# Kernel optimization log

Measured on AMD Instinct MI355X. Metric: run time of the kernel, lower is better.

The kernel has to match this reference:

```python
import jax, jax.numpy as jnp
import numpy as np

IN_CH, OUT_CH, HEADS = 256, 128, 4
DIM_HEAD = OUT_CH // HEADS  # 32 (module overrides dim_head = out_ch // heads)
R = 16  # reduce_size
EPS = 1e-5


def _conv3d(x, w, groups=1, pad=0):
    return jax.lax.conv_general_dilated(
        x, w, (1, 1, 1), [(pad, pad)] * 3,
        dimension_numbers=('NCDHW', 'OIDHW', 'NCDHW'),
        feature_group_count=groups)


def _dwsep(x, wd, wp):
    # depthwise 3x3x3 (groups=C) then pointwise 1x1x1, both bias-free
    y = _conv3d(x, wd, groups=x.shape[1], pad=1)
    return _conv3d(y, wp)


def _bn(x, g, b):
    # training-mode BatchNorm3d: biased batch stats over (N, D, H, W)
    m = x.mean(axis=(0, 2, 3, 4), keepdims=True)
    v = x.var(axis=(0, 2, 3, 4), keepdims=True)
    return (x - m) * jax.lax.rsqrt(v + EPS) * g.reshape(1, -1, 1, 1, 1) + b.reshape(1, -1, 1, 1, 1)


def _interp1(x, axis, out_len):
    in_len = x.shape[axis]
    if in_len == out_len:
        return x
    pos = jnp.arange(out_len, dtype=x.dtype) * ((in_len - 1) / (out_len - 1))  # align_corners=True
    lo = jnp.clip(jnp.floor(pos).astype(jnp.int32), 0, in_len - 1)
    hi = jnp.clip(lo + 1, 0, in_len - 1)
    w = pos - lo.astype(x.dtype)
    shp = [1] * x.ndim
    shp[axis] = out_len
    w = w.reshape(shp)
    return jnp.take(x, lo, axis=axis) * (1 - w) + jnp.take(x, hi, axis=axis) * w


def _interp3(x, size):
    for ax, s in zip((2, 3, 4), size):
        x = _interp1(x, ax, s)
    return x


def _rel_index(h, w, d):
    c = np.stack(np.meshgrid(np.arange(h), np.arange(w), np.arange(d), indexing='ij')).reshape(3, -1)
    rel = (c[:, :, None] - c[:, None, :]).transpose(1, 2, 0).astype(np.int64)
    rel[:, :, 0] += h - 1
    rel[:, :, 1] += w - 1
    rel[:, :, 0] *= 2 * h - 1
    idx = rel.sum(-1)
    # faithful to torch: negative indices wrap around the table
    return idx % ((2 * h - 1) * (2 * w - 1) * (2 * d - 1))


def _rel_bias(table, h, w, d, H, W, D, heads):
    idx = _rel_index(h, w, d)
    bias = table[idx.reshape(-1)].reshape(h, w, d, h * w, -1)
    bias = jnp.repeat(bias, H // h, axis=0)
    bias = jnp.repeat(bias, W // w, axis=1)
    bias = jnp.repeat(bias, D // d, axis=2)
    return bias.reshape(H * W * D, h * w * d, heads).transpose(2, 0, 1)[None]  # [1,heads,Nq,Nk]


def setup_inputs() -> dict:
    key = jax.random.key(0)
    ks = jax.random.split(key, 12)
    n = lambda k, s: jax.random.normal(k, s, dtype=jnp.float32)
    return {
        'x1': n(ks[0], (1, IN_CH, 8, 8, 8)),
        'x2': n(ks[1], (1, OUT_CH, 16, 16, 16)),
        'w_ch': n(ks[2], (OUT_CH, IN_CH, 1, 1, 1)) * 0.05,
        'b_ch': jnp.zeros((OUT_CH,), jnp.float32),
        'gamma_l': jnp.ones((IN_CH,), jnp.float32), 'beta_l': jnp.zeros((IN_CH,), jnp.float32),
        'gamma_h': jnp.ones((OUT_CH,), jnp.float32), 'beta_h': jnp.zeros((OUT_CH,), jnp.float32),
        'gamma2': jnp.ones((OUT_CH,), jnp.float32), 'beta2': jnp.zeros((OUT_CH,), jnp.float32),
        'kv_dw': n(ks[3], (IN_CH, 1, 3, 3, 3)) * 0.05,
        'kv_pw': n(ks[4], (2 * OUT_CH, IN_CH, 1, 1, 1)) * 0.05,
        'q_dw': n(ks[5], (OUT_CH, 1, 3, 3, 3)) * 0.05,
        'q_pw': n(ks[6], (OUT_CH, OUT_CH, 1, 1, 1)) * 0.05,
        'out_dw': n(ks[7], (OUT_CH, 1, 3, 3, 3)) * 0.05,
        'out_pw': n(ks[8], (OUT_CH, OUT_CH, 1, 1, 1)) * 0.05,
        'w_mlp': n(ks[9], (OUT_CH, OUT_CH, 1, 1, 1)) * 0.05,
        'rel_table': n(ks[10], ((2 * R - 1) ** 3, HEADS)) * 0.02,
    }


def reference(x1, x2, w_ch, b_ch, gamma_l, beta_l, gamma_h, beta_h, gamma2, beta2,
              kv_dw, kv_pw, q_dw, q_pw, out_dw, out_pw, w_mlp, rel_table):
    B, C, H, W, D = x1.shape
    _, _, HH, WH, DH = x2.shape
    residue = _interp3(_conv3d(x1, w_ch) + b_ch.reshape(1, -1, 1, 1, 1), (HH, WH, DH))
    x1n = _bn(x1, gamma_l, beta_l)
    x2n = _bn(x2, gamma_h, beta_h)
    k, v = jnp.split(_dwsep(x1n, kv_dw, kv_pw), 2, axis=1)
    q = _dwsep(x2n, q_dw, q_pw)
    if H != R:
        k = _interp3(k, (R, R, R))
        v = _interp3(v, (R, R, R))

    def heads_split(t, h, w_, d):
        # channel layout is (dim_head, heads)
        t = t.reshape(B, DIM_HEAD, HEADS, h, w_, d)
        return t.transpose(0, 2, 3, 4, 5, 1).reshape(B, HEADS, h * w_ * d, DIM_HEAD)

    qh = heads_split(q, HH, WH, DH)
    kh = heads_split(k, R, R, R)
    vh = heads_split(v, R, R, R)
    attn = jnp.einsum('bhid,bhjd->bhij', qh, kh)
    attn = attn + _rel_bias(rel_table, R, R, R, HH, WH, DH, HEADS)
    attn = jax.nn.softmax(attn * (DIM_HEAD ** -0.5), axis=-1)  # note: bias is scaled too, as in source
    o = jnp.einsum('bhij,bhjd->bhid', attn, vh)
    o = o.reshape(B, HEADS, HH, WH, DH, DIM_HEAD).transpose(0, 5, 1, 2, 3, 4).reshape(B, OUT_CH, HH, WH, DH)
    o = _dwsep(o, out_dw, out_pw)
    o = o + residue
    res2 = o
    o = jax.nn.relu(_bn(o, gamma2, beta2))
    o = _conv3d(o, w_mlp)
    return o + res2
```

## Files before the change

kernel.cpp:

```cpp
#include <hip/hip_runtime.h>
#include <hip/hip_bf16.h>

using f32x4  = __attribute__((ext_vector_type(4))) float;
using bf16x8 = __attribute__((ext_vector_type(8))) short;
using i32x4  = __attribute__((ext_vector_type(4))) int;

static constexpr float SCALE = 0.17677669529663687f;
static constexpr float L2E   = 1.4426950408889634f;
static constexpr float SL    = SCALE * L2E;

__device__ inline int cvtpk(float lo, float hi) {
  int r;
  asm("v_cvt_pk_bf16_f32 %0,%1,%2" : "=v"(r) : "v"(lo), "v"(hi));
  return r;
}

__device__ inline void bred2(float& s, float& ss) {
  #pragma unroll
  for (int off = 32; off; off >>= 1) {
    s  += __shfl_down(s, off, 64);
    ss += __shfl_down(ss, off, 64);
  }
  __shared__ float as_[4], ass_[4];
  int wid = threadIdx.x >> 6;
  if ((threadIdx.x & 63) == 0) { as_[wid] = s; ass_[wid] = ss; }
  __syncthreads();
  s  = as_[0] + as_[1] + as_[2] + as_[3];
  ss = ass_[0] + ass_[1] + ass_[2] + ass_[3];
}

__global__ __launch_bounds__(256) void bnstat_both_kernel(
    const float* __restrict__ x1, const float* __restrict__ x2,
    const float* __restrict__ gl, const float* __restrict__ bl,
    const float* __restrict__ gh, const float* __restrict__ bh,
    float* __restrict__ ab_l, float* __restrict__ ab_h) {
  int b = blockIdx.x;
  const float* src; const float *gamma, *beta; float* ab; int S, C, c;
  if (b < 256) { c = b;       src = x1 + (size_t)c * 512;  S = 512;  C = 256; gamma = gl; beta = bl; ab = ab_l; }
  else         { c = b - 256; src = x2 + (size_t)c * 4096; S = 4096; C = 128; gamma = gh; beta = bh; ab = ab_h; }
  float s = 0.f, ss = 0.f;
  for (int i = threadIdx.x; i < S; i += 256) { float v = src[i]; s += v; ss = fmaf(v, v, ss); }
  bred2(s, ss);
  if (threadIdx.x == 0) {
    float inv = 1.0f / (float)S;
    float m   = s * inv;
    float var = ss * inv - m * m;
    float a   = gamma[c] * rsqrtf(var + 1e-5f);
    ab[c]     = a;
    ab[C + c] = beta[c] - m * a;
  }
}

template<bool AFF>
__device__ inline void dw_body(
    const float* __restrict__ in, const float* __restrict__ w,
    const float* __restrict__ ab, float* __restrict__ out,
    int n, int nn, int n3, int C, int t) {
  int c = t / n3, s = t - c * n3;
  int z = s / nn, r = s - z * nn, y = r / n, x = r - y * n;
  const float* src = in + (size_t)c * n3;
  const float* wc  = w + c * 27;
  float a = 1.f, b = 0.f;
  if (AFF) { a = ab[c]; b = ab[C + c]; }
  float acc = 0.f;
  #pragma unroll
  for (int kd = 0; kd < 3; kd++) {
    int zz = z + kd - 1;
    if (zz < 0 || zz >= n) continue;
    #pragma unroll
    for (int kh = 0; kh < 3; kh++) {
      int yy = y + kh - 1;
      if (yy < 0 || yy >= n) continue;
      #pragma unroll
      for (int kw = 0; kw < 3; kw++) {
        int xx = x + kw - 1;
        if (xx < 0 || xx >= n) continue;
        float v = src[(zz * n + yy) * n + xx];
        if (AFF) v = fmaf(v, a, b);
        acc = fmaf(v, wc[kd * 9 + kh * 3 + kw], acc);
      }
    }
  }
  out[t] = acc;
}

__global__ __launch_bounds__(256) void stageA_kernel(
    const float* __restrict__ x1, const float* __restrict__ x2,
    const float* __restrict__ w_ch, const float* __restrict__ b_ch,
    const float* __restrict__ kv_dw, const float* __restrict__ q_dw,
    const float* __restrict__ ab_l, const float* __restrict__ ab_h,
    float* __restrict__ res8, float* __restrict__ kvdw, float* __restrict__ qdw) {
  int b = blockIdx.x;
  if (b < 128) {
    int oc0 = (b >> 1) * 2;
    int s   = (b & 1) * 256 + threadIdx.x;
    float a0 = 0.f, a1 = 0.f;
    const float* w0 = w_ch + (size_t)oc0 * 256;
    const float* w1 = w0 + 256;
    #pragma unroll 8
    for (int ic = 0; ic < 256; ic++) {
      float x = x1[(size_t)ic * 512 + s];
      a0 = fmaf(w0[ic], x, a0);
      a1 = fmaf(w1[ic], x, a1);
    }
    res8[(size_t)oc0 * 512 + s]       = a0 + b_ch[oc0];
    res8[(size_t)(oc0 + 1) * 512 + s] = a1 + b_ch[oc0 + 1];
  } else if (b < 640) {
    dw_body<true>(x1, kv_dw, ab_l, kvdw, 8, 64, 512, 256, (b - 128) * 256 + threadIdx.x);
  } else {
    dw_body<true>(x2, q_dw, ab_h, qdw, 16, 256, 4096, 128, (b - 640) * 256 + threadIdx.x);
  }
}

__device__ inline void icoef8(int o, int& lo, int& hi, float& w) {
  float p = (float)o * (7.0f / 15.0f);
  int l = (int)floorf(p);
  if (l > 7) l = 7;
  int h = l + 1 > 7 ? 7 : l + 1;
  w  = p - (float)l;
  lo = l; hi = h;
}

__device__ inline float trilin8(const float* __restrict__ p,
                                int z0, int z1, float wz,
                                int y0, int y1, float wy,
                                int x0, int x1, float wx) {
  float c00 = p[(z0*8+y0)*8+x0]*(1.f-wx) + p[(z0*8+y0)*8+x1]*wx;
  float c01 = p[(z0*8+y1)*8+x0]*(1.f-wx) + p[(z0*8+y1)*8+x1]*wx;
  float c10 = p[(z1*8+y0)*8+x0]*(1.f-wx) + p[(z1*8+y0)*8+x1]*wx;
  float c11 = p[(z1*8+y1)*8+x0]*(1.f-wx) + p[(z1*8+y1)*8+x1]*wx;
  float c0 = c00*(1.f-wy) + c01*wy;
  float c1 = c10*(1.f-wy) + c11*wy;
  return c0*(1.f-wz) + c1*wz;
}

__global__ __launch_bounds__(512) void stageB_kernel(
    const float* __restrict__ kvdw, const float* __restrict__ kv_pw,
    const float* __restrict__ qdw, const float* __restrict__ q_pw,
    const float* __restrict__ res8,
    unsigned short* __restrict__ Kb, unsigned short* __restrict__ Vt,
    unsigned short* __restrict__ Qpk, float* __restrict__ r16) {
  __shared__ float sm[2][512];
  int b = blockIdx.x;
  int tid = threadIdx.x;
  if (b < 128) {
    int kc0 = b * 2;
    int s = tid;
    float a0 = 0.f, a1 = 0.f;
    const float* w0 = kv_pw + (size_t)kc0 * 256;
    const float* w1 = w0 + 256;
    #pragma unroll 8
    for (int ic = 0; ic < 256; ic++) {
      float x = kvdw[(size_t)ic * 512 + s];
      a0 = fmaf(w0[ic], x, a0);
      a1 = fmaf(w1[ic], x, a1);
    }
    sm[0][s] = a0; sm[1][s] = a1;
    __syncthreads();
    #pragma unroll
    for (int r = 0; r < 16; r++) {
      int u  = r * 512 + tid;
      int cl = u >> 12, j = u & 4095;
      int z = j >> 8, y = (j >> 4) & 15, x = j & 15;
      int z0,z1,y0,y1,x0,x1; float wz,wy,wx;
      icoef8(z, z0, z1, wz); icoef8(y, y0, y1, wy); icoef8(x, x0, x1, wx);
      float val = trilin8(sm[cl], z0, z1, wz, y0, y1, wy, x0, x1, wx);
      __hip_bfloat16 bv = __float2bfloat16(val);
      unsigned short us = *reinterpret_cast<unsigned short*>(&bv);
      int kc = kc0 + cl;
      int c  = kc & 127;
      int head = c & 3, dh = c >> 2;
      if (kc < 128) Kb[((size_t)(head << 12) + j) * 32 + dh] = us;
      else          Vt[((size_t)(head * 32) + dh) * 4096 + j] = us;
    }
  } else if (b < 256) {
    int bb   = b - 128;
    int head = bb >> 5;
    int r2   = bb & 31;
    int dh0  = (r2 >> 3) * 8;
    int i    = (r2 & 7) * 512 + tid;
    float acc[8];
    #pragma unroll
    for (int e = 0; e < 8; e++) acc[e] = 0.f;
    #pragma unroll 4
    for (int ic = 0; ic < 128; ic++) {
      float x = qdw[(size_t)ic * 4096 + i];
      #pragma unroll
      for (int e = 0; e < 8; e++)
        acc[e] = fmaf(q_pw[(size_t)((dh0 + e) * 4 + head) * 128 + ic], x, acc[e]);
    }
    i32x4 pk = { cvtpk(acc[0], acc[1]), cvtpk(acc[2], acc[3]),
                 cvtpk(acc[4], acc[5]), cvtpk(acc[6], acc[7]) };
    *reinterpret_cast<i32x4*>(Qpk + ((size_t)(head << 12) + i) * 32 + dh0) = pk;
  } else {
    int t = (b - 256) * 512 + tid;
    int s = t & 4095, c = t >> 12;
    int z = s >> 8, y = (s >> 4) & 15, x = s & 15;
    int z0,z1,y0,y1,x0,x1; float wz,wy,wx;
    icoef8(z, z0, z1, wz); icoef8(y, y0, y1, wy); icoef8(x, x0, x1, wx);
    r16[t] = trilin8(res8 + c * 512, z0, z1, wz, y0, y1, wy, x0, x1, wx);
  }
}

__global__ __launch_bounds__(512, 4) void attn_mfma_kernel(
    const unsigned short* __restrict__ Qpk, const unsigned short* __restrict__ Kb,
    const unsigned short* __restrict__ Vt, const float* __restrict__ table,
    float* __restrict__ part_o, float* __restrict__ part_m, float* __restrict__ part_l) {
  __shared__ float lut[992];
  __shared__ unsigned short kvs[2][4096];

  int head = blockIdx.x >> 8;
  int rem  = blockIdx.x & 255;
  int qg   = rem >> 3;
  int ksb  = rem & 7;
  int tid  = threadIdx.x;

  for (int u = tid; u < 991; u += 512) {
    int p = (u < 15) ? (u - 15 + 29791) : (u - 15);
    lut[u] = table[p * 4 + head] * SL;
  }

  int w    = tid >> 6;
  int lane = tid & 63;
  int qrow = lane & 15;
  int g    = lane >> 4;
  int i    = qg * 128 + w * 16 + qrow;
  int iz = i >> 8, iy = (i >> 4) & 15, ix = i & 15;
  int lanebase = iz * 31 + iy + ix;

  bf16x8 qf = *(const bf16x8*)(Qpk + ((size_t)(head << 12) + i) * 32 + g * 8);

  const unsigned short* Kh = Kb + (size_t)head * 4096 * 32;
  const unsigned short* Vh = Vt + (size_t)head * 32 * 4096;

  int kt0 = ksb * 16;

  const unsigned short* src;
  size_t sstride;
  if (tid < 256) {
    int key = tid >> 2, s = tid & 3;
    int gp  = s ^ ((key >> 1) & 3);
    src = Kh + (size_t)(kt0 * 32 + key) * 32 + gp * 8;
    sstride = 32 * 32;
  } else {
    int tt = tid - 256;
    int dh = tt >> 2, s = tt & 3;
    int gp = s ^ ((dh >> 1) & 3);
    src = Vh + (size_t)dh * 4096 + kt0 * 32 + gp * 8;
    sstride = 32;
  }
  int t8 = tid * 8;

  int sw    = (qrow >> 1) & 3;
  int k0off = qrow * 32 + ((g ^ sw) * 8);
  int k1off = k0off + 512;
  int v0off = 2048 + k0off;
  int v1off = v0off + 512;

  {
    bf16x8 s0 = *(const bf16x8*)src; src += sstride;
    *(bf16x8*)(&kvs[0][t8]) = s0;
  }
  __syncthreads();

  f32x4 zero = {0.f, 0.f, 0.f, 0.f};
  f32x4 accO0 = zero, accO1 = zero;
  float m2 = -1e30f, lpart = 0.f;
  int cur = 0;

  for (int ktl = 0; ktl < 16; ktl++) {
    int kt = kt0 + ktl;
    bf16x8 stg;
    if (ktl < 15) { stg = *(const bf16x8*)src; src += sstride; }

    bf16x8 kf0 = *(const bf16x8*)(&kvs[cur][k0off]);
    bf16x8 kf1 = *(const bf16x8*)(&kvs[cur][k1off]);
    bf16x8 vf0 = *(const bf16x8*)(&kvs[cur][v0off]);
    bf16x8 vf1 = *(const bf16x8*)(&kvs[cur][v1off]);

    f32x4 accA = __builtin_amdgcn_mfma_f32_16x16x32_bf16(kf0, qf, zero, 0, 0, 0);
    f32x4 accB = __builtin_amdgcn_mfma_f32_16x16x32_bf16(kf1, qf, zero, 0, 0, 0);

    int z0 = kt >> 3, y0 = (kt << 1) & 15;
    int Cc = 495 - 31 * z0 - y0;
    const float* lp = &lut[lanebase + Cc - 4 * g - 4];
    float l0 = lp[0], l1 = lp[1], l2 = lp[2], l3 = lp[3], l4 = lp[4];

    float t0 = fmaf(accA[0], SL, l4);
    float t1 = fmaf(accA[1], SL, l3);
    float t2 = fmaf(accA[2], SL, l2);
    float t3 = fmaf(accA[3], SL, l1);
    float t4 = fmaf(accB[0], SL, l3);
    float t5 = fmaf(accB[1], SL, l2);
    float t6 = fmaf(accB[2], SL, l1);
    float t7 = fmaf(accB[3], SL, l0);

    float cm = fmaxf(fmaxf(fmaxf(t0, t1), fmaxf(t2, t3)),
                     fmaxf(fmaxf(t4, t5), fmaxf(t6, t7)));
    cm = fmaxf(cm, __shfl_xor(cm, 16, 64));
    cm = fmaxf(cm, __shfl_xor(cm, 32, 64));

    if (__any(cm > m2 + 8.f)) {
      float mn   = fmaxf(m2, cm);
      float corr = exp2f(m2 - mn);
      m2 = mn;
      lpart *= corr;
      accO0[0] *= corr; accO0[1] *= corr; accO0[2] *= corr; accO0[3] *= corr;
      accO1[0] *= corr; accO1[1] *= corr; accO1[2] *= corr; accO1[3] *= corr;
    }

    float p0 = exp2f(t0 - m2), p1 = exp2f(t1 - m2);
    float p2 = exp2f(t2 - m2), p3 = exp2f(t3 - m2);
    float p4 = exp2f(t4 - m2), p5 = exp2f(t5 - m2);
    float p6 = exp2f(t6 - m2), p7 = exp2f(t7 - m2);
    lpart += ((p0 + p1) + (p2 + p3)) + ((p4 + p5) + (p6 + p7));

    int w0 = cvtpk(p0, p1), w1 = cvtpk(p2, p3);
    int w2 = cvtpk(p4, p5), w3 = cvtpk(p6, p7);
    int srcA = ((g & 1) << 5) + qrow;
    int srcB = srcA + 16;
    int x0 = __shfl(w0, srcA, 64), x1 = __shfl(w1, srcA, 64);
    int x2 = __shfl(w2, srcA, 64), x3 = __shfl(w3, srcA, 64);
    int y0s = __shfl(w0, srcB, 64), y1s = __shfl(w1, srcB, 64);
    int y2s = __shfl(w2, srcB, 64), y3s = __shfl(w3, srcB, 64);
    bool thi = (g >> 1) != 0;
    union { i32x4 i4; bf16x8 s8; } up;
    up.i4 = (i32x4){ thi ? x2 : x0, thi ? x3 : x1,
                     thi ? y2s : y0s, thi ? y3s : y1s };

    accO0 = __builtin_amdgcn_mfma_f32_16x16x32_bf16(vf0, up.s8, accO0, 0, 0, 0);
    accO1 = __builtin_amdgcn_mfma_f32_16x16x32_bf16(vf1, up.s8, accO1, 0, 0, 0);

    if (ktl < 15) *(bf16x8*)(&kvs[cur ^ 1][t8]) = stg;
    __syncthreads();
    cur ^= 1;
  }

  float lsum = lpart + __shfl_xor(lpart, 16, 64);
  lsum += __shfl_xor(lsum, 32, 64);

  int base = head * 8 + ksb;
  if (g == 0) {
    part_m[base * 4096 + i] = m2;
    part_l[base * 4096 + i] = lsum;
  }
  #pragma unroll
  for (int r = 0; r < 4; r++) {
    part_o[(size_t)(base * 32 + 4 * g + r) * 4096 + i]      = accO0[r];
    part_o[(size_t)(base * 32 + 16 + 4 * g + r) * 4096 + i] = accO1[r];
  }
}

__global__ __launch_bounds__(256) void attn_reduce_kernel(
    const float* __restrict__ part_o, const float* __restrict__ part_m,
    const float* __restrict__ part_l, float* __restrict__ o_sp) {
  int t = blockIdx.x * 256 + threadIdx.x;
  int i = t & 4095, head = t >> 12;
  float mk[8], mx = -1e30f;
  #pragma unroll
  for (int ks = 0; ks < 8; ks++) { mk[ks] = part_m[(head*8+ks)*4096 + i]; mx = fmaxf(mx, mk[ks]); }
  float c[8], L = 0.f;
  #pragma unroll
  for (int ks = 0; ks < 8; ks++) {
    c[ks] = exp2f(mk[ks] - mx);
    L = fmaf(c[ks], part_l[(head*8+ks)*4096 + i], L);
  }
  float invL = 1.f / L;
  #pragma unroll
  for (int d = 0; d < 32; d++) {
    float acc = 0.f;
    #pragma unroll
    for (int ks = 0; ks < 8; ks++)
      acc = fmaf(c[ks], part_o[(size_t)((head*8+ks)*32 + d) * 4096 + i], acc);
    o_sp[(size_t)(d * 4 + head) * 4096 + i] = acc * invL;
  }
}

__global__ __launch_bounds__(256) void dw_out_kernel(
    const float* __restrict__ in, const float* __restrict__ w, float* __restrict__ out) {
  dw_body<false>(in, w, nullptr, out, 16, 256, 4096, 128, blockIdx.x * 256 + threadIdx.x);
}

__global__ __launch_bounds__(256) void pw_out_kernel(
    const float* __restrict__ in, const float* __restrict__ w,
    const float* __restrict__ r16, float* __restrict__ res2,
    float* __restrict__ sums) {
  __shared__ float red[4][2][2];
  int oc0 = (blockIdx.x >> 3) * 2;
  int sb  = blockIdx.x & 7;
  int s0  = (sb * 256 + threadIdx.x) * 2;
  float a00 = 0.f, a01 = 0.f, a10 = 0.f, a11 = 0.f;
  const float* w0 = w + (size_t)oc0 * 128;
  const float* w1 = w0 + 128;
  #pragma unroll 8
  for (int ic = 0; ic < 128; ic++) {
    float xa = in[(size_t)ic * 4096 + s0];
    float xb = in[(size_t)ic * 4096 + s0 + 1];
    float wv0 = w0[ic], wv1 = w1[ic];
    a00 = fmaf(wv0, xa, a00); a01 = fmaf(wv0, xb, a01);
    a10 = fmaf(wv1, xa, a10); a11 = fmaf(wv1, xb, a11);
  }
  size_t ob0 = (size_t)oc0 * 4096 + s0;
  size_t ob1 = ob0 + 4096;
  float r00 = a00 + r16[ob0],     r01 = a01 + r16[ob0 + 1];
  float r10 = a10 + r16[ob1],     r11 = a11 + r16[ob1 + 1];
  res2[ob0] = r00; res2[ob0 + 1] = r01;
  res2[ob1] = r10; res2[ob1 + 1] = r11;
  float s_0 = r00 + r01, q_0 = fmaf(r00, r00, r01 * r01);
  float s_1 = r10 + r11, q_1 = fmaf(r10, r10, r11 * r11);
  #pragma unroll
  for (int off = 32; off; off >>= 1) {
    s_0 += __shfl_down(s_0, off, 64); q_0 += __shfl_down(q_0, off, 64);
    s_1 += __shfl_down(s_1, off, 64); q_1 += __shfl_down(q_1, off, 64);
  }
  int wid = threadIdx.x >> 6;
  if ((threadIdx.x & 63) == 0) {
    red[wid][0][0] = s_0; red[wid][0][1] = q_0;
    red[wid][1][0] = s_1; red[wid][1][1] = q_1;
  }
  __syncthreads();
  if (threadIdx.x < 2) {
    int o = threadIdx.x;
    float st = red[0][o][0] + red[1][o][0] + red[2][o][0] + red[3][o][0];
    float qt = red[0][o][1] + red[1][o][1] + red[2][o][1] + red[3][o][1];
    sums[(oc0 + o) * 8 + sb]        = st;
    sums[1024 + (oc0 + o) * 8 + sb] = qt;
  }
}

__global__ __launch_bounds__(256) void pw_mlp_kernel(
    const float* __restrict__ res2, const float* __restrict__ w,
    const float* __restrict__ gamma2, const float* __restrict__ beta2,
    const float* __restrict__ sums, float* __restrict__ out) {
  __shared__ float A[128], Bb[128];
  if (threadIdx.x < 128) {
    int c = threadIdx.x;
    float s = 0.f, q = 0.f;
    #pragma unroll
    for (int sb = 0; sb < 8; sb++) { s += sums[c * 8 + sb]; q += sums[1024 + c * 8 + sb]; }
    float m   = s * (1.0f / 4096.0f);
    float var = q * (1.0f / 4096.0f) - m * m;
    float a   = gamma2[c] * rsqrtf(var + 1e-5f);
    A[c]  = a;
    Bb[c] = beta2[c] - m * a;
  }
  __syncthreads();
  int oc0 = (blockIdx.x >> 3) * 2;
  int sb  = blockIdx.x & 7;
  int s0  = (sb * 256 + threadIdx.x) * 2;
  float a00 = 0.f, a01 = 0.f, a10 = 0.f, a11 = 0.f;
  const float* w0 = w + (size_t)oc0 * 128;
  const float* w1 = w0 + 128;
  #pragma unroll 8
  for (int ic = 0; ic < 128; ic++) {
    float aa = A[ic], bb = Bb[ic];
    float xa = fmaxf(fmaf(res2[(size_t)ic * 4096 + s0], aa, bb), 0.f);
    float xb = fmaxf(fmaf(res2[(size_t)ic * 4096 + s0 + 1], aa, bb), 0.f);
    float wv0 = w0[ic], wv1 = w1[ic];
    a00 = fmaf(wv0, xa, a00); a01 = fmaf(wv0, xb, a01);
    a10 = fmaf(wv1, xa, a10); a11 = fmaf(wv1, xb, a11);
  }
  size_t ob0 = (size_t)oc0 * 4096 + s0;
  size_t ob1 = ob0 + 4096;
  out[ob0]     = a00 + res2[ob0];
  out[ob0 + 1] = a01 + res2[ob0 + 1];
  out[ob1]     = a10 + res2[ob1];
  out[ob1 + 1] = a11 + res2[ob1 + 1];
}

extern "C" void kernel_launch(void* const* d_in, const int* in_sizes, int n_in,
                              void* d_out, int out_size, void* d_ws, size_t ws_size,
                              hipStream_t stream) {
  (void)in_sizes; (void)n_in; (void)out_size; (void)ws_size;
  const float* x1      = (const float*)d_in[0];
  const float* x2      = (const float*)d_in[1];
  const float* w_ch    = (const float*)d_in[2];
  const float* b_ch    = (const float*)d_in[3];
  const float* gamma_l = (const float*)d_in[4];
  const float* beta_l  = (const float*)d_in[5];
  const float* gamma_h = (const float*)d_in[6];
  const float* beta_h  = (const float*)d_in[7];
  const float* gamma2  = (const float*)d_in[8];
  const float* beta2   = (const float*)d_in[9];
  const float* kv_dw   = (const float*)d_in[10];
  const float* kv_pw   = (const float*)d_in[11];
  const float* q_dw    = (const float*)d_in[12];
  const float* q_pw    = (const float*)d_in[13];
  const float* out_dw  = (const float*)d_in[14];
  const float* out_pw  = (const float*)d_in[15];
  const float* w_mlp   = (const float*)d_in[16];
  const float* rtab    = (const float*)d_in[17];

  float* ws = (float*)d_ws;
  float* ab_l = ws + 0;
  float* ab_h = ws + 512;
  float* sums = ws + 768;
  float* res8 = ws + 2816;
  float* kvdw = ws + 68352;
  float* qdw  = ws + 199424;
  unsigned short* Qpk = (unsigned short*)(ws + 723712);
  unsigned short* Kb  = (unsigned short*)(ws + 985856);
  unsigned short* Vt  = (unsigned short*)(ws + 1248000);
  float* r16  = ws + 1510144;
  float* o_sp = ws + 2034432;
  float* odw  = ws + 2558720;
  float* res2 = ws + 3083008;
  float* part_o = ws + 3607296;
  float* part_m = ws + 7801600;
  float* part_l = ws + 7932672;

  bnstat_both_kernel<<<384, 256, 0, stream>>>(x1, x2, gamma_l, beta_l, gamma_h, beta_h,
                                              ab_l, ab_h);
  stageA_kernel<<<2688, 256, 0, stream>>>(x1, x2, w_ch, b_ch, kv_dw, q_dw,
                                          ab_l, ab_h, res8, kvdw, qdw);
  stageB_kernel<<<1280, 512, 0, stream>>>(kvdw, kv_pw, qdw, q_pw, res8,
                                          Kb, Vt, Qpk, r16);
  attn_mfma_kernel<<<1024, 512, 0, stream>>>(Qpk, Kb, Vt, rtab,
                                             part_o, part_m, part_l);
  attn_reduce_kernel<<<64, 256, 0, stream>>>(part_o, part_m, part_l, o_sp);
  dw_out_kernel<<<2048, 256, 0, stream>>>(o_sp, out_dw, odw);
  pw_out_kernel<<<512, 256, 0, stream>>>(odw, out_pw, r16, res2, sums);
  pw_mlp_kernel<<<512, 256, 0, stream>>>(res2, w_mlp, gamma2, beta2, sums, (float*)d_out);
}
```

Measured before the change: 112.5 us.

## Permute K key layout so P feeds PV MFMA directly without shuffles

Stores K with a permuted key order inside each 32-key tile so that the softmax probabilities computed per lane already sit in the A-operand layout of the PV MFMA. This removes eight cross-lane shuffles and selects per tile, and swaps operand order so the output accumulator is transposed (query-major across lanes). The row-max correction now needs four shuffles to redistribute per-query correction factors, but only on the rare rescale path. Partial outputs are written as 16-byte vector stores instead of scalar strided stores.

Measured after the change: 109.1 us. -3.0%, faster.

```diff
diff --git a/kernel.cpp b/kernel.cpp
--- a/kernel.cpp
+++ b/kernel.cpp
@@ -170,8 +170,13 @@
       int kc = kc0 + cl;
       int c  = kc & 127;
       int head = c & 3, dh = c >> 2;
-      if (kc < 128) Kb[((size_t)(head << 12) + j) * 32 + dh] = us;
-      else          Vt[((size_t)(head * 32) + dh) * 4096 + j] = us;
+      if (kc < 128) {
+        int k  = j & 31;
+        int jp = (j & ~31) | (((k >> 3) << 2) + (k & 3) + ((k & 4) ? 16 : 0));
+        Kb[((size_t)(head << 12) + jp) * 32 + dh] = us;
+      } else {
+        Vt[((size_t)(head * 32) + dh) * 4096 + j] = us;
+      }
     }
   } else if (b < 256) {
     int bb   = b - 128;
@@ -227,6 +232,7 @@
   int i    = qg * 128 + w * 16 + qrow;
   int iz = i >> 8, iy = (i >> 4) & 15, ix = i & 15;
   int lanebase = iz * 31 + iy + ix;
+  int gof = ((g >= 2) ? 15 : 0) - 8 * g;
 
   bf16x8 qf = *(const bf16x8*)(Qpk + ((size_t)(head << 12) + i) * 32 + g * 8);
 
@@ -283,17 +289,18 @@
 
     int z0 = kt >> 3, y0 = (kt << 1) & 15;
     int Cc = 495 - 31 * z0 - y0;
-    const float* lp = &lut[lanebase + Cc - 4 * g - 4];
-    float l0 = lp[0], l1 = lp[1], l2 = lp[2], l3 = lp[3], l4 = lp[4];
-
-    float t0 = fmaf(accA[0], SL, l4);
-    float t1 = fmaf(accA[1], SL, l3);
-    float t2 = fmaf(accA[2], SL, l2);
-    float t3 = fmaf(accA[3], SL, l1);
-    float t4 = fmaf(accB[0], SL, l3);
-    float t5 = fmaf(accB[1], SL, l2);
-    float t6 = fmaf(accB[2], SL, l1);
-    float t7 = fmaf(accB[3], SL, l0);
+    const float* lp = &lut[lanebase + Cc + gof - 7];
+    float b0 = lp[0], b1 = lp[1], b2 = lp[2], b3 = lp[3];
+    float b4 = lp[4], b5 = lp[5], b6 = lp[6], b7 = lp[7];
+
+    float t0 = fmaf(accA[0], SL, b7);
+    float t1 = fmaf(accA[1], SL, b6);
+    float t2 = fmaf(accA[2], SL, b5);
+    float t3 = fmaf(accA[3], SL, b4);
+    float t4 = fmaf(accB[0], SL, b3);
+    float t5 = fmaf(accB[1], SL, b2);
+    float t6 = fmaf(accB[2], SL, b1);
+    float t7 = fmaf(accB[3], SL, b0);
 
     float cm = fmaxf(fmaxf(fmaxf(t0, t1), fmaxf(t2, t3)),
                      fmaxf(fmaxf(t4, t5), fmaxf(t6, t7)));
@@ -305,8 +312,12 @@
       float corr = exp2f(m2 - mn);
       m2 = mn;
       lpart *= corr;
-      accO0[0] *= corr; accO0[1] *= corr; accO0[2] *= corr; accO0[3] *= corr;
-      accO1[0] *= corr; accO1[1] *= corr; accO1[2] *= corr; accO1[3] *= corr;
+      float c0 = __shfl(corr, g * 4 + 0, 64);
+      float c1 = __shfl(corr, g * 4 + 1, 64);
+      float c2 = __shfl(corr, g * 4 + 2, 64);
+      float c3 = __shfl(corr, g * 4 + 3, 64);
+      accO0[0] *= c0; accO0[1] *= c1; accO0[2] *= c2; accO0[3] *= c3;
+      accO1[0] *= c0; accO1[1] *= c1; accO1[2] *= c2; accO1[3] *= c3;
     }
 
     float p0 = exp2f(t0 - m2), p1 = exp2f(t1 - m2);
@@ -315,21 +326,12 @@
     float p6 = exp2f(t6 - m2), p7 = exp2f(t7 - m2);
     lpart += ((p0 + p1) + (p2 + p3)) + ((p4 + p5) + (p6 + p7));
 
-    int w0 = cvtpk(p0, p1), w1 = cvtpk(p2, p3);
-    int w2 = cvtpk(p4, p5), w3 = cvtpk(p6, p7);
-    int srcA = ((g & 1) << 5) + qrow;
-    int srcB = srcA + 16;
-    int x0 = __shfl(w0, srcA, 64), x1 = __shfl(w1, srcA, 64);
-    int x2 = __shfl(w2, srcA, 64), x3 = __shfl(w3, srcA, 64);
-    int y0s = __shfl(w0, srcB, 64), y1s = __shfl(w1, srcB, 64);
-    int y2s = __shfl(w2, srcB, 64), y3s = __shfl(w3, srcB, 64);
-    bool thi = (g >> 1) != 0;
-    union { i32x4 i4; bf16x8 s8; } up;
-    up.i4 = (i32x4){ thi ? x2 : x0, thi ? x3 : x1,
-                     thi ? y2s : y0s, thi ? y3s : y1s };
-
-    accO0 = __builtin_amdgcn_mfma_f32_16x16x32_bf16(vf0, up.s8, accO0, 0, 0, 0);
-    accO1 = __builtin_amdgcn_mfma_f32_16x16x32_bf16(vf1, up.s8, accO1, 0, 0, 0);
+    union { i32x4 i4; bf16x8 s8; } pa;
+    pa.i4 = (i32x4){ cvtpk(p0, p1), cvtpk(p2, p3),
+                     cvtpk(p4, p5), cvtpk(p6, p7) };
+
+    accO0 = __builtin_amdgcn_mfma_f32_16x16x32_bf16(pa.s8, vf0, accO0, 0, 0, 0);
+    accO1 = __builtin_amdgcn_mfma_f32_16x16x32_bf16(pa.s8, vf1, accO1, 0, 0, 0);
 
     if (ktl < 15) *(bf16x8*)(&kvs[cur ^ 1][t8]) = stg;
     __syncthreads();
@@ -344,11 +346,9 @@
     part_m[base * 4096 + i] = m2;
     part_l[base * 4096 + i] = lsum;
   }
-  #pragma unroll
-  for (int r = 0; r < 4; r++) {
-    part_o[(size_t)(base * 32 + 4 * g + r) * 4096 + i]      = accO0[r];
-    part_o[(size_t)(base * 32 + 16 + 4 * g + r) * 4096 + i] = accO1[r];
-  }
+  int i0 = qg * 128 + w * 16 + g * 4;
+  *(f32x4*)&part_o[(size_t)(base * 32 + qrow) * 4096 + i0]      = accO0;
+  *(f32x4*)&part_o[(size_t)(base * 32 + 16 + qrow) * 4096 + i0] = accO1;
 }
 
 __global__ __launch_bounds__(256) void attn_reduce_kernel(
```
